# Performance work log

Hardware: AMD Instinct MI355X
Metric: run time of the kernel (lower is better)

Reference implementation:

```python
import jax, jax.numpy as jnp
import numpy as np

SCALE = 1.0  # module scale
# dropout is treated as identity (eval mode / deterministic reference)

def setup_inputs() -> dict:
    key = jax.random.key(0)
    k_x, k_w, k1, k2, k3 = jax.random.split(key, 5)
    B, S, D = 4, 4096, 1280
    x = jax.random.normal(k_x, (B, S, D), dtype=jnp.float32)
    W = jax.random.normal(k_w, (D, D), dtype=jnp.float32) * 0.02  # linear.weight [out, in]
    # kron factors are initialized to identity in the module; perturb slightly
    # so the rotation is non-trivial for correctness testing.
    kron_1 = jnp.eye(4, dtype=jnp.float32) + 0.01 * jax.random.normal(k1, (4, 4), dtype=jnp.float32)
    kron_2 = jnp.eye(8, dtype=jnp.float32) + 0.01 * jax.random.normal(k2, (8, 8), dtype=jnp.float32)
    kron_3 = jnp.eye(40, dtype=jnp.float32) + 0.01 * jax.random.normal(k3, (40, 40), dtype=jnp.float32)
    return {"x": x, "W": W, "kron_1": kron_1, "kron_2": kron_2, "kron_3": kron_3}

def reference(x, W, kron_1, kron_2, kron_3):
    # rotate_matrix = kron(kron(k1, k2), k3)  -> [in, in] = [1280, 1280]
    R = jnp.kron(jnp.kron(kron_1, kron_2), kron_3)
    # rotated_weight = (R @ W^T)^T ; F.linear(x, rotated_weight) = x @ (R @ W^T)
    rotated_weight = (R @ W.T).T  # [out, in]
    out = jnp.einsum('bsd,od->bso', x, rotated_weight)
    return out * SCALE
```

## Files before the change

kernel.cpp:

```cpp
#include <hip/hip_runtime.h>
#include <hip/hip_bf16.h>
#include <stdint.h>

typedef __bf16 bf16x8 __attribute__((ext_vector_type(8)));
typedef float floatx4 __attribute__((ext_vector_type(4)));

__device__ __forceinline__ void async_copy16(void* lds, const void* g) {
    __builtin_amdgcn_global_load_lds(
        (const __attribute__((address_space(1))) unsigned int*)g,
        (__attribute__((address_space(3))) unsigned int*)lds,
        16, 0, 0);
}

__global__ __launch_bounds__(256)
void prep(const float* __restrict__ x,
          const float* __restrict__ W,
          const float* __restrict__ K1,
          const float* __restrict__ K2,
          const float* __restrict__ K3,
          __hip_bfloat16* __restrict__ x_bf,
          __hip_bfloat16* __restrict__ Wrot,
          int nConv) {
    const int tid = threadIdx.x;

    if ((int)blockIdx.x < nConv) {
        const size_t i = ((size_t)blockIdx.x * 256 + tid) * 8;
        const float4 a = *(const float4*)(x + i);
        const float4 b = *(const float4*)(x + i + 4);
        bf16x8 v;
        v[0] = (__bf16)a.x; v[1] = (__bf16)a.y; v[2] = (__bf16)a.z; v[3] = (__bf16)a.w;
        v[4] = (__bf16)b.x; v[5] = (__bf16)b.y; v[6] = (__bf16)b.z; v[7] = (__bf16)b.w;
        *(bf16x8*)((__bf16*)x_bf + i) = v;
        return;
    }

    const int o = blockIdx.x - nConv;
    __shared__ __align__(16) float w0[1280];
    __shared__ __align__(16) float t1[1280];
    __shared__ __align__(16) float k3s[1600];
    __shared__ float k2s[64];
    __shared__ float k1s[16];

    for (int i = tid; i < 1280; i += 256) w0[i] = W[o * 1280 + i];
    for (int i = tid; i < 1600; i += 256) k3s[i] = K3[i];
    if (tid < 64) k2s[tid] = K2[tid];
    if (tid < 16) k1s[tid] = K1[tid];
    __syncthreads();

    for (int i = tid; i < 1280; i += 256) {
        const int p = i / 40, d3 = i % 40;
        const float4* w4 = (const float4*)(w0 + p * 40);
        const float4* k4 = (const float4*)(k3s + d3 * 40);
        float acc = 0.f;
#pragma unroll
        for (int t = 0; t < 10; ++t) {
            const float4 a = w4[t], b = k4[t];
            acc += a.x * b.x + a.y * b.y + a.z * b.z + a.w * b.w;
        }
        t1[i] = acc;
    }
    __syncthreads();

    for (int i = tid; i < 1280; i += 256) {
        const int d3 = i % 40, pd = i / 40;
        const int k1 = pd >> 3, d2 = pd & 7;
        float acc = 0.f;
#pragma unroll
        for (int k2 = 0; k2 < 8; ++k2) acc += t1[(k1 * 8 + k2) * 40 + d3] * k2s[d2 * 8 + k2];
        w0[i] = acc;
    }
    __syncthreads();

    for (int i = tid; i < 1280; i += 256) {
        const int d3 = i % 40, pd = i / 40;
        const int d1 = pd >> 3, d2 = pd & 7;
        float acc = 0.f;
#pragma unroll
        for (int k1 = 0; k1 < 4; ++k1) acc += w0[(k1 * 8 + d2) * 40 + d3] * k1s[d1 * 4 + k1];
        Wrot[(size_t)o * 1280 + i] = __float2bfloat16(acc);
    }
}

#define BM 256
#define BN 320
#define BK 64
#define AGRAN 2048
#define BGRAN 2560

__global__ __launch_bounds__(512, 2)
void gemm_bt(const __hip_bfloat16* __restrict__ A,
             const __hip_bfloat16* __restrict__ B,
             float* __restrict__ C,
             int M, int N, int K) {
    __shared__ bf16x8 As[2][AGRAN];
    __shared__ bf16x8 Bs[2][BGRAN];

    const int tid  = threadIdx.x;
    const int wave = tid >> 6;
    const int lane = tid & 63;
    const int q    = lane >> 4;
    const int r16  = lane & 15;
    const int wm   = wave >> 2;
    const int wn   = wave & 3;

    const int nTilesN = N / BN;
    const int chunkM  = (M / BM) >> 3;
    const int xcd = blockIdx.x & 7;
    const int s   = blockIdx.x >> 3;
    const int bm  = xcd * chunkM + s / nTilesN;
    const int bn  = s % nTilesN;
    const int tileM = bm * BM, tileN = bn * BN;

    uint32_t aoff[4], boff[5];
#pragma unroll
    for (int c = 0; c < 4; ++c) {
        const int g = c * 512 + tid;
        const int m = g >> 3, kv = (g & 7) ^ (m & 7);
        aoff[c] = (uint32_t)(((tileM + m) * K + kv * 8) * 2);
    }
#pragma unroll
    for (int c = 0; c < 5; ++c) {
        const int g = c * 512 + tid;
        const int m = g >> 3, kv = (g & 7) ^ (m & 7);
        boff[c] = (uint32_t)(((tileN + m) * K + kv * 8) * 2);
    }
    const char* Abase = (const char*)A;
    const char* Bbase = (const char*)B;

    int ai[8], bi[5];
#pragma unroll
    for (int i = 0; i < 8; ++i) {
        const int m = wm * 128 + i * 16 + r16;
        ai[i] = m * 8 + (q ^ (m & 7));
    }
#pragma unroll
    for (int j = 0; j < 5; ++j) {
        const int n = wn * 80 + j * 16 + r16;
        bi[j] = n * 8 + (q ^ (n & 7));
    }

    floatx4 acc[8][5];
#pragma unroll
    for (int i = 0; i < 8; ++i)
#pragma unroll
        for (int j = 0; j < 5; ++j) acc[i][j] = (floatx4){0.f, 0.f, 0.f, 0.f};

    const int nk = K / BK;

#pragma unroll
    for (int c = 0; c < 4; ++c)
        async_copy16(&As[0][c * 512 + wave * 64], Abase + aoff[c]);
#pragma unroll
    for (int c = 0; c < 5; ++c)
        async_copy16(&Bs[0][c * 512 + wave * 64], Bbase + boff[c]);
    asm volatile("s_waitcnt vmcnt(0)" ::: "memory");
    __builtin_amdgcn_s_barrier();

    bf16x8 bf0[5], bf1[5], af[4];

    for (int t = 0; t < nk; ++t) {
        const int cur = t & 1, nxt = cur ^ 1;
        const uint32_t kb = (uint32_t)((t + 1) * BK * 2);
        const bool hn = (t + 1 < nk);

#pragma unroll
        for (int i = 0; i < 4; ++i) af[i] = As[cur][ai[i]];
#pragma unroll
        for (int j = 0; j < 5; ++j) bf0[j] = Bs[cur][bi[j]];
        if (hn) {
            async_copy16(&As[nxt][0 * 512 + wave * 64], Abase + aoff[0] + kb);
            async_copy16(&As[nxt][2 * 512 + wave * 64], Abase + aoff[2] + kb);
            async_copy16(&Bs[nxt][0 * 512 + wave * 64], Bbase + boff[0] + kb);
        }
        __builtin_amdgcn_sched_barrier(0);
        __builtin_amdgcn_s_barrier();
        __builtin_amdgcn_sched_barrier(0);
        __builtin_amdgcn_s_setprio(1);
#pragma unroll
        for (int j = 0; j < 5; ++j)
#pragma unroll
            for (int i = 0; i < 4; ++i)
                acc[i][j] = __builtin_amdgcn_mfma_f32_16x16x32_bf16(
                    af[i], bf0[j], acc[i][j], 0, 0, 0);
        __builtin_amdgcn_s_setprio(0);
        __builtin_amdgcn_sched_barrier(0);
        __builtin_amdgcn_s_barrier();

#pragma unroll
        for (int i = 0; i < 4; ++i) af[i] = As[cur][ai[i] ^ 4];
#pragma unroll
        for (int j = 0; j < 5; ++j) bf1[j] = Bs[cur][bi[j] ^ 4];
        if (hn) {
            async_copy16(&Bs[nxt][1 * 512 + wave * 64], Bbase + boff[1] + kb);
            async_copy16(&Bs[nxt][2 * 512 + wave * 64], Bbase + boff[2] + kb);
            asm volatile("s_waitcnt vmcnt(5)" ::: "memory");
        } else {
            asm volatile("s_waitcnt vmcnt(0)" ::: "memory");
        }
        __builtin_amdgcn_sched_barrier(0);
        __builtin_amdgcn_s_barrier();
        __builtin_amdgcn_sched_barrier(0);
        __builtin_amdgcn_s_setprio(1);
#pragma unroll
        for (int j = 0; j < 5; ++j)
#pragma unroll
            for (int i = 0; i < 4; ++i)
                acc[i][j] = __builtin_amdgcn_mfma_f32_16x16x32_bf16(
                    af[i], bf1[j], acc[i][j], 0, 0, 0);
        __builtin_amdgcn_s_setprio(0);
        __builtin_amdgcn_sched_barrier(0);
        __builtin_amdgcn_s_barrier();

#pragma unroll
        for (int i = 0; i < 4; ++i) af[i] = As[cur][ai[4 + i]];
        if (hn) {
            async_copy16(&Bs[nxt][3 * 512 + wave * 64], Bbase + boff[3] + kb);
            async_copy16(&Bs[nxt][4 * 512 + wave * 64], Bbase + boff[4] + kb);
        }
        __builtin_amdgcn_sched_barrier(0);
        __builtin_amdgcn_s_barrier();
        __builtin_amdgcn_sched_barrier(0);
        __builtin_amdgcn_s_setprio(1);
#pragma unroll
        for (int i = 0; i < 4; ++i)
#pragma unroll
            for (int j = 0; j < 5; ++j)
                acc[4 + i][j] = __builtin_amdgcn_mfma_f32_16x16x32_bf16(
                    af[i], bf0[j], acc[4 + i][j], 0, 0, 0);
        __builtin_amdgcn_s_setprio(0);
        __builtin_amdgcn_sched_barrier(0);
        __builtin_amdgcn_s_barrier();

#pragma unroll
        for (int i = 0; i < 4; ++i) af[i] = As[cur][ai[4 + i] ^ 4];
        if (hn) {
            async_copy16(&As[nxt][1 * 512 + wave * 64], Abase + aoff[1] + kb);
            async_copy16(&As[nxt][3 * 512 + wave * 64], Abase + aoff[3] + kb);
            asm volatile("s_waitcnt vmcnt(2)" ::: "memory");
        }
        __builtin_amdgcn_sched_barrier(0);
        __builtin_amdgcn_s_barrier();
        __builtin_amdgcn_sched_barrier(0);
        __builtin_amdgcn_s_setprio(1);
#pragma unroll
        for (int i = 0; i < 4; ++i)
#pragma unroll
            for (int j = 0; j < 5; ++j)
                acc[4 + i][j] = __builtin_amdgcn_mfma_f32_16x16x32_bf16(
                    af[i], bf1[j], acc[4 + i][j], 0, 0, 0);
        __builtin_amdgcn_s_setprio(0);
        __builtin_amdgcn_sched_barrier(0);
        __builtin_amdgcn_s_barrier();
    }

#pragma unroll
    for (int i = 0; i < 8; ++i) {
#pragma unroll
        for (int j = 0; j < 5; ++j) {
            const int col = tileN + wn * 80 + j * 16 + r16;
#pragma unroll
            for (int r = 0; r < 4; ++r) {
                const int row = tileM + wm * 128 + i * 16 + q * 4 + r;
                C[(size_t)row * N + col] = acc[i][j][r];
            }
        }
    }
}

extern "C" void kernel_launch(void* const* d_in, const int* in_sizes, int n_in,
                              void* d_out, int out_size, void* d_ws, size_t ws_size,
                              hipStream_t stream) {
    const float* x  = (const float*)d_in[0];
    const float* W  = (const float*)d_in[1];
    const float* K1 = (const float*)d_in[2];
    const float* K2 = (const float*)d_in[3];
    const float* K3 = (const float*)d_in[4];
    float* out = (float*)d_out;

    const int D = 1280;
    const int M = in_sizes[0] / D;
    const int N = D, K = D;

    __hip_bfloat16* x_bf = (__hip_bfloat16*)d_ws;
    __hip_bfloat16* Wrot = x_bf + (size_t)M * K;

    const int nConv = (M * K) / (256 * 8);
    prep<<<nConv + D, 256, 0, stream>>>(x, W, K1, K2, K3, x_bf, Wrot, nConv);
    gemm_bt<<<(M / BM) * (N / BN), 512, 0, stream>>>(x_bf, Wrot, out, M, N, K);
}
```

Before: 219.8 us.

## Fuse fp32-to-bf16 conversion of x into GEMM A-tile loads

The separate pass that converted x to bf16 in the prep kernel is removed. The GEMM now reads fp32 x straight into registers, converts to bf16 and writes the swizzled A tiles to LDS itself, while B keeps its async direct-to-LDS copies. This drops a full write and re-read of the bf16 copy of x. In exchange, each A element is read as fp32 once for every N tile (four tiles), so A traffic goes up, and the A path now needs register staging plus a full vmcnt/lgkmcnt wait at the end of each iteration, which may reduce overlap.

```diff
diff --git a/kernel.cpp b/kernel.cpp
--- a/kernel.cpp
+++ b/kernel.cpp
@@ -12,29 +12,21 @@
         16, 0, 0);
 }
 
+__device__ __forceinline__ bf16x8 cvt8(float4 u, float4 v) {
+    bf16x8 r;
+    r[0] = (__bf16)u.x; r[1] = (__bf16)u.y; r[2] = (__bf16)u.z; r[3] = (__bf16)u.w;
+    r[4] = (__bf16)v.x; r[5] = (__bf16)v.y; r[6] = (__bf16)v.z; r[7] = (__bf16)v.w;
+    return r;
+}
+
 __global__ __launch_bounds__(256)
-void prep(const float* __restrict__ x,
-          const float* __restrict__ W,
+void prep(const float* __restrict__ W,
           const float* __restrict__ K1,
           const float* __restrict__ K2,
           const float* __restrict__ K3,
-          __hip_bfloat16* __restrict__ x_bf,
-          __hip_bfloat16* __restrict__ Wrot,
-          int nConv) {
+          __hip_bfloat16* __restrict__ Wrot) {
     const int tid = threadIdx.x;
-
-    if ((int)blockIdx.x < nConv) {
-        const size_t i = ((size_t)blockIdx.x * 256 + tid) * 8;
-        const float4 a = *(const float4*)(x + i);
-        const float4 b = *(const float4*)(x + i + 4);
-        bf16x8 v;
-        v[0] = (__bf16)a.x; v[1] = (__bf16)a.y; v[2] = (__bf16)a.z; v[3] = (__bf16)a.w;
-        v[4] = (__bf16)b.x; v[5] = (__bf16)b.y; v[6] = (__bf16)b.z; v[7] = (__bf16)b.w;
-        *(bf16x8*)((__bf16*)x_bf + i) = v;
-        return;
-    }
-
-    const int o = blockIdx.x - nConv;
+    const int o = blockIdx.x;
     __shared__ __align__(16) float w0[1280];
     __shared__ __align__(16) float t1[1280];
     __shared__ __align__(16) float k3s[1600];
@@ -88,7 +80,7 @@
 #define BGRAN 2560
 
 __global__ __launch_bounds__(512, 2)
-void gemm_bt(const __hip_bfloat16* __restrict__ A,
+void gemm_bt(const float* __restrict__ X,
              const __hip_bfloat16* __restrict__ B,
              float* __restrict__ C,
              int M, int N, int K) {
@@ -116,7 +108,7 @@
     for (int c = 0; c < 4; ++c) {
         const int g = c * 512 + tid;
         const int m = g >> 3, kv = (g & 7) ^ (m & 7);
-        aoff[c] = (uint32_t)(((tileM + m) * K + kv * 8) * 2);
+        aoff[c] = (uint32_t)(((tileM + m) * K + kv * 8) * 4);
     }
 #pragma unroll
     for (int c = 0; c < 5; ++c) {
@@ -124,8 +116,8 @@
         const int m = g >> 3, kv = (g & 7) ^ (m & 7);
         boff[c] = (uint32_t)(((tileN + m) * K + kv * 8) * 2);
     }
-    const char* Abase = (const char*)A;
-    const char* Bbase = (const char*)B;
+    const char* Xb = (const char*)X;
+    const char* Bb = (const char*)B;
 
     int ai[8], bi[5];
 #pragma unroll
@@ -147,20 +139,29 @@
 
     const int nk = K / BK;
 
-#pragma unroll
-    for (int c = 0; c < 4; ++c)
-        async_copy16(&As[0][c * 512 + wave * 64], Abase + aoff[c]);
-#pragma unroll
-    for (int c = 0; c < 5; ++c)
-        async_copy16(&Bs[0][c * 512 + wave * 64], Bbase + boff[c]);
-    asm volatile("s_waitcnt vmcnt(0)" ::: "memory");
-    __builtin_amdgcn_s_barrier();
+    {
+        float4 p0, p1;
+#pragma unroll
+        for (int c = 0; c < 5; ++c)
+            async_copy16(&Bs[0][c * 512 + wave * 64], Bb + boff[c]);
+#pragma unroll
+        for (int c = 0; c < 4; ++c) {
+            p0 = *(const float4*)(Xb + aoff[c]);
+            p1 = *(const float4*)(Xb + aoff[c] + 16);
+            As[0][c * 512 + tid] = cvt8(p0, p1);
+        }
+        asm volatile("s_waitcnt vmcnt(0)" ::: "memory");
+        asm volatile("s_waitcnt lgkmcnt(0)" ::: "memory");
+        __builtin_amdgcn_s_barrier();
+    }
 
     bf16x8 bf0[5], bf1[5], af[4];
+    float4 a0, a1, a2, a3, a4, a5, a6, a7;
 
     for (int t = 0; t < nk; ++t) {
         const int cur = t & 1, nxt = cur ^ 1;
-        const uint32_t kb = (uint32_t)((t + 1) * BK * 2);
+        const uint32_t kbA = (uint32_t)((t + 1) * BK * 4);
+        const uint32_t kbB = (uint32_t)((t + 1) * BK * 2);
         const bool hn = (t + 1 < nk);
 
 #pragma unroll
@@ -168,9 +169,11 @@
 #pragma unroll
         for (int j = 0; j < 5; ++j) bf0[j] = Bs[cur][bi[j]];
         if (hn) {
-            async_copy16(&As[nxt][0 * 512 + wave * 64], Abase + aoff[0] + kb);
-            async_copy16(&As[nxt][2 * 512 + wave * 64], Abase + aoff[2] + kb);
-            async_copy16(&Bs[nxt][0 * 512 + wave * 64], Bbase + boff[0] + kb);
+            a0 = *(const float4*)(Xb + aoff[0] + kbA);
+            a1 = *(const float4*)(Xb + aoff[0] + kbA + 16);
+            a2 = *(const float4*)(Xb + aoff[1] + kbA);
+            a3 = *(const float4*)(Xb + aoff[1] + kbA + 16);
+            async_copy16(&Bs[nxt][0 * 512 + wave * 64], Bb + boff[0] + kbB);
         }
         __builtin_amdgcn_sched_barrier(0);
         __builtin_amdgcn_s_barrier();
@@ -191,11 +194,14 @@
 #pragma unroll
         for (int j = 0; j < 5; ++j) bf1[j] = Bs[cur][bi[j] ^ 4];
         if (hn) {
-            async_copy16(&Bs[nxt][1 * 512 + wave * 64], Bbase + boff[1] + kb);
-            async_copy16(&Bs[nxt][2 * 512 + wave * 64], Bbase + boff[2] + kb);
-            asm volatile("s_waitcnt vmcnt(5)" ::: "memory");
-        } else {
-            asm volatile("s_waitcnt vmcnt(0)" ::: "memory");
+            a4 = *(const float4*)(Xb + aoff[2] + kbA);
+            a5 = *(const float4*)(Xb + aoff[2] + kbA + 16);
+            a6 = *(const float4*)(Xb + aoff[3] + kbA);
+            a7 = *(const float4*)(Xb + aoff[3] + kbA + 16);
+            async_copy16(&Bs[nxt][1 * 512 + wave * 64], Bb + boff[1] + kbB);
+            async_copy16(&Bs[nxt][2 * 512 + wave * 64], Bb + boff[2] + kbB);
+            As[nxt][0 * 512 + tid] = cvt8(a0, a1);
+            As[nxt][1 * 512 + tid] = cvt8(a2, a3);
         }
         __builtin_amdgcn_sched_barrier(0);
         __builtin_amdgcn_s_barrier();
@@ -214,8 +220,10 @@
 #pragma unroll
         for (int i = 0; i < 4; ++i) af[i] = As[cur][ai[4 + i]];
         if (hn) {
-            async_copy16(&Bs[nxt][3 * 512 + wave * 64], Bbase + boff[3] + kb);
-            async_copy16(&Bs[nxt][4 * 512 + wave * 64], Bbase + boff[4] + kb);
+            async_copy16(&Bs[nxt][3 * 512 + wave * 64], Bb + boff[3] + kbB);
+            async_copy16(&Bs[nxt][4 * 512 + wave * 64], Bb + boff[4] + kbB);
+            As[nxt][2 * 512 + tid] = cvt8(a4, a5);
+            As[nxt][3 * 512 + tid] = cvt8(a6, a7);
         }
         __builtin_amdgcn_sched_barrier(0);
         __builtin_amdgcn_s_barrier();
@@ -233,11 +241,6 @@
 
 #pragma unroll
         for (int i = 0; i < 4; ++i) af[i] = As[cur][ai[4 + i] ^ 4];
-        if (hn) {
-            async_copy16(&As[nxt][1 * 512 + wave * 64], Abase + aoff[1] + kb);
-            async_copy16(&As[nxt][3 * 512 + wave * 64], Abase + aoff[3] + kb);
-            asm volatile("s_waitcnt vmcnt(2)" ::: "memory");
-        }
         __builtin_amdgcn_sched_barrier(0);
         __builtin_amdgcn_s_barrier();
         __builtin_amdgcn_sched_barrier(0);
@@ -249,6 +252,11 @@
                 acc[4 + i][j] = __builtin_amdgcn_mfma_f32_16x16x32_bf16(
                     af[i], bf1[j], acc[4 + i][j], 0, 0, 0);
         __builtin_amdgcn_s_setprio(0);
+        __builtin_amdgcn_sched_barrier(0);
+        if (hn) {
+            asm volatile("s_waitcnt vmcnt(0)" ::: "memory");
+            asm volatile("s_waitcnt lgkmcnt(0)" ::: "memory");
+        }
         __builtin_amdgcn_sched_barrier(0);
         __builtin_amdgcn_s_barrier();
     }
@@ -281,10 +289,8 @@
     const int M = in_sizes[0] / D;
     const int N = D, K = D;
 
-    __hip_bfloat16* x_bf = (__hip_bfloat16*)d_ws;
-    __hip_bfloat16* Wrot = x_bf + (size_t)M * K;
-
-    const int nConv = (M * K) / (256 * 8);
-    prep<<<nConv + D, 256, 0, stream>>>(x, W, K1, K2, K3, x_bf, Wrot, nConv);
-    gemm_bt<<<(M / BM) * (N / BN), 512, 0, stream>>>(x_bf, Wrot, out, M, N, K);
-}
+    __hip_bfloat16* Wrot = (__hip_bfloat16*)d_ws;
+
+    prep<<<D, 256, 0, stream>>>(W, K1, K2, K3, Wrot);
+    gemm_bt<<<(M / BM) * (N / BN), 512, 0, stream>>>(x, Wrot, out, M, N, K);
+}
```

Measured after the change: 288.4 us. 1.31x slower.

## Simplify GEMM main loop to bulk prefetch and a single barrier per K-step

Applied to the files above, without the earlier changes.

Replaces the four-phase interleaved schedule, which split global-to-LDS prefetches across sub-phases with a barrier around each MFMA group, with a simpler loop. Each K-tile now issues all next-tile async copies up front. It then runs two full 8x5 MFMA phases over the two K halves and ends with one vmcnt(0) wait and a single barrier. This removes many workgroup barriers and scheduling fences per iteration. In exchange it gives up the staggered load/compute interleaving and raises live fragment registers.

```diff
diff --git a/kernel.cpp b/kernel.cpp
--- a/kernel.cpp
+++ b/kernel.cpp
@@ -156,101 +156,56 @@
     asm volatile("s_waitcnt vmcnt(0)" ::: "memory");
     __builtin_amdgcn_s_barrier();
 
-    bf16x8 bf0[5], bf1[5], af[4];
-
     for (int t = 0; t < nk; ++t) {
         const int cur = t & 1, nxt = cur ^ 1;
         const uint32_t kb = (uint32_t)((t + 1) * BK * 2);
         const bool hn = (t + 1 < nk);
 
-#pragma unroll
-        for (int i = 0; i < 4; ++i) af[i] = As[cur][ai[i]];
+        if (hn) {
+#pragma unroll
+            for (int c = 0; c < 4; ++c)
+                async_copy16(&As[nxt][c * 512 + wave * 64], Abase + aoff[c] + kb);
+#pragma unroll
+            for (int c = 0; c < 5; ++c)
+                async_copy16(&Bs[nxt][c * 512 + wave * 64], Bbase + boff[c] + kb);
+        }
+
+        bf16x8 af0[8], bf0[5];
+#pragma unroll
+        for (int i = 0; i < 8; ++i) af0[i] = As[cur][ai[i]];
 #pragma unroll
         for (int j = 0; j < 5; ++j) bf0[j] = Bs[cur][bi[j]];
+
+        __builtin_amdgcn_s_setprio(1);
+#pragma unroll
+        for (int i = 0; i < 8; ++i)
+#pragma unroll
+            for (int j = 0; j < 5; ++j)
+                acc[i][j] = __builtin_amdgcn_mfma_f32_16x16x32_bf16(
+                    af0[i], bf0[j], acc[i][j], 0, 0, 0);
+        __builtin_amdgcn_s_setprio(0);
+
+        bf16x8 af1[8], bf1[5];
+#pragma unroll
+        for (int i = 0; i < 8; ++i) af1[i] = As[cur][ai[i] ^ 4];
+#pragma unroll
+        for (int j = 0; j < 5; ++j) bf1[j] = Bs[cur][bi[j] ^ 4];
+
+        __builtin_amdgcn_s_setprio(1);
+#pragma unroll
+        for (int i = 0; i < 8; ++i)
+#pragma unroll
+            for (int j = 0; j < 5; ++j)
+                acc[i][j] = __builtin_amdgcn_mfma_f32_16x16x32_bf16(
+                    af1[i], bf1[j], acc[i][j], 0, 0, 0);
+        __builtin_amdgcn_s_setprio(0);
+
         if (hn) {
-            async_copy16(&As[nxt][0 * 512 + wave * 64], Abase + aoff[0] + kb);
-            async_copy16(&As[nxt][2 * 512 + wave * 64], Abase + aoff[2] + kb);
-            async_copy16(&Bs[nxt][0 * 512 + wave * 64], Bbase + boff[0] + kb);
-        }
-        __builtin_amdgcn_sched_barrier(0);
-        __builtin_amdgcn_s_barrier();
-        __builtin_amdgcn_sched_barrier(0);
-        __builtin_amdgcn_s_setprio(1);
-#pragma unroll
-        for (int j = 0; j < 5; ++j)
-#pragma unroll
-            for (int i = 0; i < 4; ++i)
-                acc[i][j] = __builtin_amdgcn_mfma_f32_16x16x32_bf16(
-                    af[i], bf0[j], acc[i][j], 0, 0, 0);
-        __builtin_amdgcn_s_setprio(0);
-        __builtin_amdgcn_sched_barrier(0);
-        __builtin_amdgcn_s_barrier();
-
-#pragma unroll
-        for (int i = 0; i < 4; ++i) af[i] = As[cur][ai[i] ^ 4];
-#pragma unroll
-        for (int j = 0; j < 5; ++j) bf1[j] = Bs[cur][bi[j] ^ 4];
-        if (hn) {
-            async_copy16(&Bs[nxt][1 * 512 + wave * 64], Bbase + boff[1] + kb);
-            async_copy16(&Bs[nxt][2 * 512 + wave * 64], Bbase + boff[2] + kb);
-            asm volatile("s_waitcnt vmcnt(5)" ::: "memory");
-        } else {
             asm volatile("s_waitcnt vmcnt(0)" ::: "memory");
-        }
-        __builtin_amdgcn_sched_barrier(0);
-        __builtin_amdgcn_s_barrier();
-        __builtin_amdgcn_sched_barrier(0);
-        __builtin_amdgcn_s_setprio(1);
-#pragma unroll
-        for (int j = 0; j < 5; ++j)
-#pragma unroll
-            for (int i = 0; i < 4; ++i)
-                acc[i][j] = __builtin_amdgcn_mfma_f32_16x16x32_bf16(
-                    af[i], bf1[j], acc[i][j], 0, 0, 0);
-        __builtin_amdgcn_s_setprio(0);
-        __builtin_amdgcn_sched_barrier(0);
-        __builtin_amdgcn_s_barrier();
-
-#pragma unroll
-        for (int i = 0; i < 4; ++i) af[i] = As[cur][ai[4 + i]];
-        if (hn) {
-            async_copy16(&Bs[nxt][3 * 512 + wave * 64], Bbase + boff[3] + kb);
-            async_copy16(&Bs[nxt][4 * 512 + wave * 64], Bbase + boff[4] + kb);
-        }
-        __builtin_amdgcn_sched_barrier(0);
-        __builtin_amdgcn_s_barrier();
-        __builtin_amdgcn_sched_barrier(0);
-        __builtin_amdgcn_s_setprio(1);
-#pragma unroll
-        for (int i = 0; i < 4; ++i)
-#pragma unroll
-            for (int j = 0; j < 5; ++j)
-                acc[4 + i][j] = __builtin_amdgcn_mfma_f32_16x16x32_bf16(
-                    af[i], bf0[j], acc[4 + i][j], 0, 0, 0);
-        __builtin_amdgcn_s_setprio(0);
-        __builtin_amdgcn_sched_barrier(0);
-        __builtin_amdgcn_s_barrier();
-
-#pragma unroll
-        for (int i = 0; i < 4; ++i) af[i] = As[cur][ai[4 + i] ^ 4];
-        if (hn) {
-            async_copy16(&As[nxt][1 * 512 + wave * 64], Abase + aoff[1] + kb);
-            async_copy16(&As[nxt][3 * 512 + wave * 64], Abase + aoff[3] + kb);
-            asm volatile("s_waitcnt vmcnt(2)" ::: "memory");
-        }
-        __builtin_amdgcn_sched_barrier(0);
-        __builtin_amdgcn_s_barrier();
-        __builtin_amdgcn_sched_barrier(0);
-        __builtin_amdgcn_s_setprio(1);
-#pragma unroll
-        for (int i = 0; i < 4; ++i)
-#pragma unroll
-            for (int j = 0; j < 5; ++j)
-                acc[4 + i][j] = __builtin_amdgcn_mfma_f32_16x16x32_bf16(
-                    af[i], bf1[j], acc[4 + i][j], 0, 0, 0);
-        __builtin_amdgcn_s_setprio(0);
-        __builtin_amdgcn_sched_barrier(0);
-        __builtin_amdgcn_s_barrier();
+            __builtin_amdgcn_sched_barrier(0);
+            __builtin_amdgcn_s_barrier();
+            __builtin_amdgcn_sched_barrier(0);
+        }
     }
 
 #pragma unroll
```

Result: slower. 225.7 us (+2.6%).

## Software-pipeline LDS fragment reads one phase ahead of MFMA blocks

Applied to the files above, without the earlier changes.

Restructures the GEMM main loop so the LDS fragment loads for the next MFMA phase are issued before the current phase's MFMAs, using separate register sets (afA..afD). The next tile's first fragments are prefetched before the last MFMA block of each iteration. This cuts barriers from eight to about three per k-step and aims to hide LDS latency behind matrix-core work. The extra fragment registers raise VGPR pressure, and the single full vmcnt(0) wait near the end of each iteration may expose global-load latency.

```diff
diff --git a/kernel.cpp b/kernel.cpp
--- a/kernel.cpp
+++ b/kernel.cpp
@@ -156,101 +156,98 @@
     asm volatile("s_waitcnt vmcnt(0)" ::: "memory");
     __builtin_amdgcn_s_barrier();
 
-    bf16x8 bf0[5], bf1[5], af[4];
+    bf16x8 bf0[5], bf1[5], afA[4], afB[4], afC[4], afD[4];
+#pragma unroll
+    for (int i = 0; i < 4; ++i) afA[i] = As[0][ai[i]];
+#pragma unroll
+    for (int j = 0; j < 5; ++j) bf0[j] = Bs[0][bi[j]];
 
     for (int t = 0; t < nk; ++t) {
         const int cur = t & 1, nxt = cur ^ 1;
         const uint32_t kb = (uint32_t)((t + 1) * BK * 2);
         const bool hn = (t + 1 < nk);
 
-#pragma unroll
-        for (int i = 0; i < 4; ++i) af[i] = As[cur][ai[i]];
-#pragma unroll
-        for (int j = 0; j < 5; ++j) bf0[j] = Bs[cur][bi[j]];
         if (hn) {
             async_copy16(&As[nxt][0 * 512 + wave * 64], Abase + aoff[0] + kb);
             async_copy16(&As[nxt][2 * 512 + wave * 64], Abase + aoff[2] + kb);
             async_copy16(&Bs[nxt][0 * 512 + wave * 64], Bbase + boff[0] + kb);
         }
+#pragma unroll
+        for (int i = 0; i < 4; ++i) afB[i] = As[cur][ai[i] ^ 4];
+#pragma unroll
+        for (int j = 0; j < 5; ++j) bf1[j] = Bs[cur][bi[j] ^ 4];
+        __builtin_amdgcn_sched_barrier(0);
+        __builtin_amdgcn_s_setprio(1);
+#pragma unroll
+        for (int j = 0; j < 5; ++j)
+#pragma unroll
+            for (int i = 0; i < 4; ++i)
+                acc[i][j] = __builtin_amdgcn_mfma_f32_16x16x32_bf16(
+                    afA[i], bf0[j], acc[i][j], 0, 0, 0);
+        __builtin_amdgcn_s_setprio(0);
         __builtin_amdgcn_sched_barrier(0);
         __builtin_amdgcn_s_barrier();
         __builtin_amdgcn_sched_barrier(0);
-        __builtin_amdgcn_s_setprio(1);
-#pragma unroll
-        for (int j = 0; j < 5; ++j)
-#pragma unroll
-            for (int i = 0; i < 4; ++i)
-                acc[i][j] = __builtin_amdgcn_mfma_f32_16x16x32_bf16(
-                    af[i], bf0[j], acc[i][j], 0, 0, 0);
-        __builtin_amdgcn_s_setprio(0);
-        __builtin_amdgcn_sched_barrier(0);
-        __builtin_amdgcn_s_barrier();
-
-#pragma unroll
-        for (int i = 0; i < 4; ++i) af[i] = As[cur][ai[i] ^ 4];
-#pragma unroll
-        for (int j = 0; j < 5; ++j) bf1[j] = Bs[cur][bi[j] ^ 4];
+
         if (hn) {
             async_copy16(&Bs[nxt][1 * 512 + wave * 64], Bbase + boff[1] + kb);
             async_copy16(&Bs[nxt][2 * 512 + wave * 64], Bbase + boff[2] + kb);
-            asm volatile("s_waitcnt vmcnt(5)" ::: "memory");
-        } else {
-            asm volatile("s_waitcnt vmcnt(0)" ::: "memory");
-        }
+        }
+#pragma unroll
+        for (int i = 0; i < 4; ++i) afC[i] = As[cur][ai[4 + i]];
+        __builtin_amdgcn_sched_barrier(0);
+        __builtin_amdgcn_s_setprio(1);
+#pragma unroll
+        for (int j = 0; j < 5; ++j)
+#pragma unroll
+            for (int i = 0; i < 4; ++i)
+                acc[i][j] = __builtin_amdgcn_mfma_f32_16x16x32_bf16(
+                    afB[i], bf1[j], acc[i][j], 0, 0, 0);
+        __builtin_amdgcn_s_setprio(0);
         __builtin_amdgcn_sched_barrier(0);
         __builtin_amdgcn_s_barrier();
         __builtin_amdgcn_sched_barrier(0);
-        __builtin_amdgcn_s_setprio(1);
-#pragma unroll
-        for (int j = 0; j < 5; ++j)
-#pragma unroll
-            for (int i = 0; i < 4; ++i)
-                acc[i][j] = __builtin_amdgcn_mfma_f32_16x16x32_bf16(
-                    af[i], bf1[j], acc[i][j], 0, 0, 0);
-        __builtin_amdgcn_s_setprio(0);
-        __builtin_amdgcn_sched_barrier(0);
-        __builtin_amdgcn_s_barrier();
-
-#pragma unroll
-        for (int i = 0; i < 4; ++i) af[i] = As[cur][ai[4 + i]];
+
         if (hn) {
             async_copy16(&Bs[nxt][3 * 512 + wave * 64], Bbase + boff[3] + kb);
             async_copy16(&Bs[nxt][4 * 512 + wave * 64], Bbase + boff[4] + kb);
-        }
-        __builtin_amdgcn_sched_barrier(0);
-        __builtin_amdgcn_s_barrier();
-        __builtin_amdgcn_sched_barrier(0);
-        __builtin_amdgcn_s_setprio(1);
-#pragma unroll
-        for (int i = 0; i < 4; ++i)
-#pragma unroll
-            for (int j = 0; j < 5; ++j)
-                acc[4 + i][j] = __builtin_amdgcn_mfma_f32_16x16x32_bf16(
-                    af[i], bf0[j], acc[4 + i][j], 0, 0, 0);
-        __builtin_amdgcn_s_setprio(0);
-        __builtin_amdgcn_sched_barrier(0);
-        __builtin_amdgcn_s_barrier();
-
-#pragma unroll
-        for (int i = 0; i < 4; ++i) af[i] = As[cur][ai[4 + i] ^ 4];
-        if (hn) {
             async_copy16(&As[nxt][1 * 512 + wave * 64], Abase + aoff[1] + kb);
             async_copy16(&As[nxt][3 * 512 + wave * 64], Abase + aoff[3] + kb);
-            asm volatile("s_waitcnt vmcnt(2)" ::: "memory");
-        }
-        __builtin_amdgcn_sched_barrier(0);
-        __builtin_amdgcn_s_barrier();
-        __builtin_amdgcn_sched_barrier(0);
-        __builtin_amdgcn_s_setprio(1);
-#pragma unroll
-        for (int i = 0; i < 4; ++i)
-#pragma unroll
-            for (int j = 0; j < 5; ++j)
+        }
+#pragma unroll
+        for (int i = 0; i < 4; ++i) afD[i] = As[cur][ai[4 + i] ^ 4];
+        __builtin_amdgcn_sched_barrier(0);
+        __builtin_amdgcn_s_setprio(1);
+#pragma unroll
+        for (int j = 0; j < 5; ++j)
+#pragma unroll
+            for (int i = 0; i < 4; ++i)
                 acc[4 + i][j] = __builtin_amdgcn_mfma_f32_16x16x32_bf16(
-                    af[i], bf1[j], acc[4 + i][j], 0, 0, 0);
-        __builtin_amdgcn_s_setprio(0);
-        __builtin_amdgcn_sched_barrier(0);
-        __builtin_amdgcn_s_barrier();
+                    afC[i], bf0[j], acc[4 + i][j], 0, 0, 0);
+        __builtin_amdgcn_s_setprio(0);
+        __builtin_amdgcn_sched_barrier(0);
+
+        if (hn) {
+            asm volatile("s_waitcnt lgkmcnt(0)" ::: "memory");
+            asm volatile("s_waitcnt vmcnt(0)" ::: "memory");
+            __builtin_amdgcn_sched_barrier(0);
+            __builtin_amdgcn_s_barrier();
+            __builtin_amdgcn_sched_barrier(0);
+#pragma unroll
+            for (int i = 0; i < 4; ++i) afA[i] = As[nxt][ai[i]];
+#pragma unroll
+            for (int j = 0; j < 5; ++j) bf0[j] = Bs[nxt][bi[j]];
+            __builtin_amdgcn_sched_barrier(0);
+        }
+        __builtin_amdgcn_s_setprio(1);
+#pragma unroll
+        for (int j = 0; j < 5; ++j)
+#pragma unroll
+            for (int i = 0; i < 4; ++i)
+                acc[4 + i][j] = __builtin_amdgcn_mfma_f32_16x16x32_bf16(
+                    afD[i], bf1[j], acc[4 + i][j], 0, 0, 0);
+        __builtin_amdgcn_s_setprio(0);
+        __builtin_amdgcn_sched_barrier(0);
     }
 
 #pragma unroll
```

Measured after the change: 271.2 us. 23.4% more time.
